# Kernel tuning notes

Hardware: AMD Instinct MI355X
Metric: run time of the kernel (lower is better)

## Reference

```python
import jax, jax.numpy as jnp
import numpy as np

B, N, H = 2, 2048, 1024
NUM_HEADS, HEAD_DIM = 16, 64
SCALE = HEAD_DIM ** -0.5


def setup_inputs() -> dict:
    key = jax.random.key(0)
    ks = jax.random.split(key, 9)
    hidden_states = jax.random.normal(ks[0], (B, N, H), dtype=jnp.float32)
    # ancestor-only mask: lower-triangular incl. diagonal (chain tree)
    tree_mask = jnp.tril(jnp.ones((N, N), dtype=jnp.int32))
    s = H ** -0.5
    Wq = jax.random.normal(ks[1], (H, NUM_HEADS * HEAD_DIM), dtype=jnp.float32) * s
    Wk = jax.random.normal(ks[2], (H, NUM_HEADS * HEAD_DIM), dtype=jnp.float32) * s
    Wv = jax.random.normal(ks[3], (H, NUM_HEADS * HEAD_DIM), dtype=jnp.float32) * s
    Wo = jax.random.normal(ks[4], (NUM_HEADS * HEAD_DIM, H), dtype=jnp.float32) * s
    bq = jnp.zeros((NUM_HEADS * HEAD_DIM,), dtype=jnp.float32)
    bk = jnp.zeros((NUM_HEADS * HEAD_DIM,), dtype=jnp.float32)
    bv = jnp.zeros((NUM_HEADS * HEAD_DIM,), dtype=jnp.float32)
    bo = jnp.zeros((H,), dtype=jnp.float32)
    return {"hidden_states": hidden_states, "tree_mask": tree_mask,
            "Wq": Wq, "bq": bq, "Wk": Wk, "bk": bk,
            "Wv": Wv, "bv": bv, "Wo": Wo, "bo": bo}


def reference(hidden_states, tree_mask, Wq, bq, Wk, bk, Wv, bv, Wo, bo):
    b, n, _ = hidden_states.shape
    q = (hidden_states @ Wq + bq).reshape(b, n, NUM_HEADS, HEAD_DIM)
    k = (hidden_states @ Wk + bk).reshape(b, n, NUM_HEADS, HEAD_DIM)
    v = (hidden_states @ Wv + bv).reshape(b, n, NUM_HEADS, HEAD_DIM)
    # scores: [b, heads, n, n]
    scores = jnp.einsum('bqhd,bkhd->bhqk', q, k) * SCALE
    neg_inf = jnp.finfo(scores.dtype).min
    scores = jnp.where(tree_mask[None, None, :, :] == 0, neg_inf, scores)
    attn = jax.nn.softmax(scores, axis=-1)  # dropout p=0.0 -> identity
    out = jnp.einsum('bhqk,bkhd->bqhd', attn, v).reshape(b, n, NUM_HEADS * HEAD_DIM)
    return out @ Wo + bo
```

## Files before the change

kernel.cpp:

```cpp
#include <hip/hip_runtime.h>
#include <hip/hip_bf16.h>
#include <stdint.h>

typedef unsigned short u16;
typedef short short8 __attribute__((ext_vector_type(8)));
typedef float f32x4 __attribute__((ext_vector_type(4)));
typedef u16 u16x4 __attribute__((ext_vector_type(4)));

#define SCLOG 0.18033688011112042f

static __device__ __forceinline__ u16 f2bf(float f) {
  unsigned u = __float_as_uint(f);
  unsigned rnd = 0x7fffu + ((u >> 16) & 1u);
  return (u16)((u + rnd) >> 16);
}

static __device__ __forceinline__ unsigned pk_bf16(float a, float b) {
  unsigned r;
  asm("v_cvt_pk_bf16_f32 %0, %1, %2" : "=v"(r) : "v"(a), "v"(b));
  return r;
}

static __device__ __forceinline__ void gload_lds16(const void* g, void* l) {
  __builtin_amdgcn_global_load_lds(
      (const __attribute__((address_space(1))) unsigned int*)g,
      (__attribute__((address_space(3))) unsigned int*)l, 16, 0, 0);
}

__global__ __launch_bounds__(256) void cvt_hs_kernel(const float4* __restrict__ src,
                                                     u16x4* __restrict__ dst) {
  int i = blockIdx.x * 256 + threadIdx.x;
  float4 v = src[i];
  u16x4 o;
  o[0] = f2bf(v.x); o[1] = f2bf(v.y); o[2] = f2bf(v.z); o[3] = f2bf(v.w);
  dst[i] = o;
}

__global__ __launch_bounds__(256) void cvt_transpose_kernel(
    const float* __restrict__ Wq, const float* __restrict__ Wk,
    const float* __restrict__ Wv, const float* __restrict__ Wo,
    u16* __restrict__ WT) {
  __shared__ float tile[32][33];
  const int z = blockIdx.z;
  const float* src = (z == 0) ? Wq : (z == 1) ? Wk : (z == 2) ? Wv : Wo;
  u16* dst = WT + (size_t)z * 1024 * 1024;
  const int row0 = blockIdx.y * 32, col0 = blockIdx.x * 32;
  const int tx = threadIdx.x, ty = threadIdx.y;
#pragma unroll
  for (int i = 0; i < 4; ++i)
    tile[ty + i * 8][tx] = src[(size_t)(row0 + ty + i * 8) * 1024 + col0 + tx];
  __syncthreads();
#pragma unroll
  for (int i = 0; i < 4; ++i) {
    int r = ty + i * 8;
    dst[(size_t)(col0 + r) * 1024 + row0 + tx] = f2bf(tile[tx][r]);
  }
}

__global__ __launch_bounds__(256) void mask_bits_kernel(const int* __restrict__ mask,
                                                        unsigned long long* __restrict__ bits) {
  int gw = blockIdx.x * 4 + (threadIdx.x >> 6);
  int lane = threadIdx.x & 63;
  int q = gw >> 5, w = gw & 31;
  int mv = mask[(size_t)q * 2048 + w * 64 + lane];
  unsigned long long bal = __ballot(mv != 0);
  if (lane == 0) bits[(size_t)q * 32 + w] = bal;
}

__global__ __launch_bounds__(256) void gemm_qkv_kernel(
    const u16* __restrict__ X, const u16* __restrict__ WT,
    const float* __restrict__ bq, const float* __restrict__ bk, const float* __restrict__ bv,
    u16* __restrict__ Qb, u16* __restrict__ Kb, u16* __restrict__ Vb) {
  __shared__ u16 As[128 * 32];
  __shared__ u16 Bs[128 * 32];
  const int tid = threadIdx.x;
  const int lane = tid & 63, wid = tid >> 6;
  const int l15 = lane & 15, lg = lane >> 4;
  const int n0 = blockIdx.x * 128, m0 = blockIdx.y * 128;
  const int wr = wid >> 1, wc = wid & 1;

  f32x4 acc[4][4] = {};

  for (int kt = 0; kt < 32; ++kt) {
    __syncthreads();
#pragma unroll
    for (int p = 0; p < 2; ++p) {
      const int c = p * 256 + tid;
      const int r = c >> 2, ch = c & 3;
      gload_lds16(X + (size_t)(m0 + r) * 1024 + kt * 32 + ch * 8,
                  &As[(p * 256 + wid * 64) * 8]);
      gload_lds16(WT + (size_t)(n0 + r) * 1024 + kt * 32 + ch * 8,
                  &Bs[(p * 256 + wid * 64) * 8]);
    }
    __syncthreads();
    short8 af[4], bfr[4];
#pragma unroll
    for (int i = 0; i < 4; ++i) {
      af[i] = *reinterpret_cast<const short8*>(&As[(wr * 64 + i * 16 + l15) * 32 + lg * 8]);
      bfr[i] = *reinterpret_cast<const short8*>(&Bs[(wc * 64 + i * 16 + l15) * 32 + lg * 8]);
    }
#pragma unroll
    for (int i = 0; i < 4; ++i)
#pragma unroll
      for (int j = 0; j < 4; ++j)
        acc[i][j] = __builtin_amdgcn_mfma_f32_16x16x32_bf16(af[i], bfr[j], acc[i][j], 0, 0, 0);
  }

#pragma unroll
  for (int j = 0; j < 4; ++j) {
    const int n = n0 + wc * 64 + j * 16 + l15;
    const float bias = (n < 1024) ? bq[n] : (n < 2048) ? bk[n - 1024] : bv[n - 2048];
    const float scl = (n < 1024) ? SCLOG : 1.0f;
    u16* dst = (n < 1024) ? Qb : (n < 2048) ? Kb : Vb;
    const int nl = n & 1023;
    const int hh = nl >> 6, d = nl & 63;
#pragma unroll
    for (int i = 0; i < 4; ++i) {
#pragma unroll
      for (int r = 0; r < 4; ++r) {
        const int m = m0 + wr * 64 + i * 16 + lg * 4 + r;
        const int bb = m >> 11, t = m & 2047;
        dst[((size_t)(bb * 16 + hh) * 2048 + t) * 64 + d] = f2bf((acc[i][j][r] + bias) * scl);
      }
    }
  }
}

__global__ __launch_bounds__(256) void transpose_v_kernel(const u16* __restrict__ Vb,
                                                          u16* __restrict__ VT) {
  __shared__ u16 tile[64][68];
  const int tid = threadIdx.x;
  const int tt = blockIdx.x & 31;
  const int bh = blockIdx.x >> 5;
  const size_t base = (size_t)bh * 2048 * 64;
  const int t0 = tt * 64;
#pragma unroll
  for (int p = 0; p < 2; ++p) {
    int i = p * 256 + tid;
    int row = i >> 3, ch = i & 7;
    *reinterpret_cast<short8*>(&tile[row][ch * 8]) =
        *reinterpret_cast<const short8*>(Vb + base + (size_t)(t0 + row) * 64 + ch * 8);
  }
  __syncthreads();
#pragma unroll
  for (int p = 0; p < 2; ++p) {
    int i = p * 256 + tid;
    int d = i >> 3, ch = i & 7;
    short8 v;
#pragma unroll
    for (int j = 0; j < 8; ++j) v[j] = tile[ch * 8 + j][d];
    *reinterpret_cast<short8*>(VT + base + (size_t)d * 2048 + t0 + ch * 8) = v;
  }
}

struct AttnState {
  f32x4 O[4];
  float m, l;
  short8 qf0, qf1;
};

static __device__ __forceinline__ void attn_tile(
    AttnState& st, const u16* __restrict__ Kb_, const u16* __restrict__ Vb_,
    u16* __restrict__ pwave, unsigned long long w,
    int l15, int lg, int slg) {
  f32x4 sT[4] = {};
  __builtin_amdgcn_s_setprio(1);
#pragma unroll
  for (int dc = 0; dc < 2; ++dc) {
    const short8 qv = dc ? st.qf1 : st.qf0;
#pragma unroll
    for (int sub = 0; sub < 4; ++sub) {
      const short8 kf = *reinterpret_cast<const short8*>(
          &Kb_[dc * 2048 + (sub * 16 + l15) * 32 + slg]);
      sT[sub] = __builtin_amdgcn_mfma_f32_16x16x32_bf16(kf, qv, sT[sub], 0, 0, 0);
    }
  }
  __builtin_amdgcn_s_setprio(0);

  float pm = -3e38f;
  if (__all(w == ~0ull)) {
#pragma unroll
    for (int sub = 0; sub < 4; ++sub)
#pragma unroll
      for (int r = 0; r < 4; ++r) pm = fmaxf(pm, sT[sub][r]);
  } else {
    const unsigned mlo = (unsigned)w, mhi = (unsigned)(w >> 32);
#pragma unroll
    for (int sub = 0; sub < 4; ++sub) {
      const unsigned f = ((sub & 2) ? mhi : mlo) >> ((sub & 1) * 16 + lg * 4);
#pragma unroll
      for (int r = 0; r < 4; ++r) {
        const float val = ((f >> r) & 1u) ? sT[sub][r] : -1e30f;
        sT[sub][r] = val;
        pm = fmaxf(pm, val);
      }
    }
  }
  pm = fmaxf(pm, __shfl_xor(pm, 16));
  pm = fmaxf(pm, __shfl_xor(pm, 32));
  if (!__all(pm - st.m <= 8.f)) {
    const float mn = fmaxf(st.m, pm);
    const float al = exp2f(st.m - mn);
    st.m = mn;
    st.l *= al;
#pragma unroll
    for (int dt = 0; dt < 4; ++dt) st.O[dt] *= al;
  }

  float lsum = 0.f;
#pragma unroll
  for (int kc = 0; kc < 2; ++kc) {
#pragma unroll
    for (int s2 = 0; s2 < 2; ++s2) {
      const int sub = kc * 2 + s2;
      const float e0 = exp2f(sT[sub][0] - st.m);
      const float e1 = exp2f(sT[sub][1] - st.m);
      const float e2 = exp2f(sT[sub][2] - st.m);
      const float e3 = exp2f(sT[sub][3] - st.m);
      lsum += (e0 + e1) + (e2 + e3);
      uint2 pk;
      pk.x = pk_bf16(e0, e1);
      pk.y = pk_bf16(e2, e3);
      *reinterpret_cast<uint2*>(&pwave[l15 * 40 + s2 * 16 + lg * 4]) = pk;
    }
    const short8 pf = *reinterpret_cast<const short8*>(&pwave[l15 * 40 + lg * 8]);
    __builtin_amdgcn_s_setprio(1);
#pragma unroll
    for (int dt = 0; dt < 4; ++dt) {
      const short8 vf = *reinterpret_cast<const short8*>(
          &Vb_[kc * 2048 + (dt * 16 + l15) * 32 + slg]);
      st.O[dt] = __builtin_amdgcn_mfma_f32_16x16x32_bf16(vf, pf, st.O[dt], 0, 0, 0);
    }
    __builtin_amdgcn_s_setprio(0);
  }
  lsum += __shfl_xor(lsum, 16);
  lsum += __shfl_xor(lsum, 32);
  st.l += lsum;
}

__global__ __launch_bounds__(256, 4) void attn_kernel(
    const u16* __restrict__ Q, const u16* __restrict__ K, const u16* __restrict__ VT,
    const unsigned long long* __restrict__ MB, u16* __restrict__ AO) {
  __shared__ u16 K_lds[2][4096];
  __shared__ u16 V_lds[2][4096];
  __shared__ u16 p_lds[4][16][40];
  __shared__ unsigned actA_s, actB_s;

  const int tid = threadIdx.x;
  const int wid = tid >> 6, lane = tid & 63;
  const int l15 = lane & 15, lg = lane >> 4;

  const int qp = blockIdx.x;
  const int qA_t = qp, qB_t = 31 - qp;
  const int h = blockIdx.y;
  const int b = blockIdx.z;
  const size_t bh_off = ((size_t)(b * 16 + h)) * 2048 * 64;

  if (tid == 0) { actA_s = 0; actB_s = 0; }
  __syncthreads();
  {
    const int ktc = tid & 31, qg = tid >> 5;
    unsigned long long orA = 0, orB = 0;
#pragma unroll
    for (int i = 0; i < 8; ++i) {
      orA |= MB[(size_t)(qA_t * 64 + qg * 8 + i) * 32 + ktc];
      orB |= MB[(size_t)(qB_t * 64 + qg * 8 + i) * 32 + ktc];
    }
    if (orA) atomicOr(&actA_s, 1u << ktc);
    if (orB) atomicOr(&actB_s, 1u << ktc);
  }

  const int qa = qA_t * 64 + wid * 16 + l15;
  const int qb = qB_t * 64 + wid * 16 + l15;

  AttnState stA, stB;
  {
    const short8* qpA = reinterpret_cast<const short8*>(Q + bh_off + (size_t)qa * 64);
    const short8* qpB = reinterpret_cast<const short8*>(Q + bh_off + (size_t)qb * 64);
    stA.qf0 = qpA[lg]; stA.qf1 = qpA[4 + lg];
    stB.qf0 = qpB[lg]; stB.qf1 = qpB[4 + lg];
#pragma unroll
    for (int dt = 0; dt < 4; ++dt) { stA.O[dt] = f32x4{}; stB.O[dt] = f32x4{}; }
    stA.m = -3e38f; stA.l = 0.f;
    stB.m = -3e38f; stB.l = 0.f;
  }

  const int slg = (lg ^ ((l15 >> 1) & 3)) * 8;

  int offK[2], offV[2], ldsi[2];
#pragma unroll
  for (int p = 0; p < 2; ++p) {
    const int i = wid * 128 + p * 64 + lane;
    const int pc = i >> 8, row = (i >> 2) & 63, lgc = i & 3;
    const int lgs = lgc ^ ((i >> 3) & 3);
    offK[p] = row * 64 + pc * 32 + lgs * 8;
    offV[p] = row * 2048 + pc * 32 + lgs * 8;
    ldsi[p] = (wid * 128 + p * 64) * 8;
  }
  const u16* Kg = K + bh_off;
  const u16* Vg = VT + bh_off;
  u16* pwave = &p_lds[wid][0][0];

  __syncthreads();
  const unsigned actA = actA_s, actB = actB_s;
  unsigned rem = actA | actB;
  int buf = 0;

#define STAGE_TILE(bb, ktv)                                        \
  do {                                                             \
    const u16* ksrc_ = Kg + (ktv) * 64 * 64;                       \
    const u16* vsrc_ = Vg + (ktv) * 64;                            \
    _Pragma("unroll") for (int p_ = 0; p_ < 2; ++p_) {             \
      gload_lds16(ksrc_ + offK[p_], &K_lds[bb][ldsi[p_]]);         \
      gload_lds16(vsrc_ + offV[p_], &V_lds[bb][ldsi[p_]]);         \
    }                                                              \
  } while (0)

  if (rem) {
    int kt = __ffs(rem) - 1;
    unsigned long long wA_cur = MB[(size_t)qa * 32 + kt];
    unsigned long long wB_cur = MB[(size_t)qb * 32 + kt];
    STAGE_TILE(0, kt);
    __syncthreads();

    while (true) {
      rem &= rem - 1;
      int ktn = -1;
      unsigned long long wA_next = 0, wB_next = 0;
      if (rem) {
        ktn = __ffs(rem) - 1;
        wA_next = MB[(size_t)qa * 32 + ktn];
        wB_next = MB[(size_t)qb * 32 + ktn];
        STAGE_TILE(buf ^ 1, ktn);
      }

      if ((actB >> kt) & 1u)
        attn_tile(stB, &K_lds[buf][0], &V_lds[buf][0], pwave, wB_cur, l15, lg, slg);
      if ((actA >> kt) & 1u)
        attn_tile(stA, &K_lds[buf][0], &V_lds[buf][0], pwave, wA_cur, l15, lg, slg);

      if (ktn < 0) break;
      __syncthreads();
      buf ^= 1;
      kt = ktn;
      wA_cur = wA_next;
      wB_cur = wB_next;
    }
  }
#undef STAGE_TILE

  {
    const float invA = (stA.l > 0.f) ? (1.0f / stA.l) : 0.f;
    u16* dstA = AO + ((size_t)(b * 2048 + qa)) * 1024 + h * 64;
#pragma unroll
    for (int dt = 0; dt < 4; ++dt) {
      uint2 pk;
      pk.x = pk_bf16(stA.O[dt][0] * invA, stA.O[dt][1] * invA);
      pk.y = pk_bf16(stA.O[dt][2] * invA, stA.O[dt][3] * invA);
      *reinterpret_cast<uint2*>(dstA + dt * 16 + lg * 4) = pk;
    }
    const float invB = (stB.l > 0.f) ? (1.0f / stB.l) : 0.f;
    u16* dstB = AO + ((size_t)(b * 2048 + qb)) * 1024 + h * 64;
#pragma unroll
    for (int dt = 0; dt < 4; ++dt) {
      uint2 pk;
      pk.x = pk_bf16(stB.O[dt][0] * invB, stB.O[dt][1] * invB);
      pk.y = pk_bf16(stB.O[dt][2] * invB, stB.O[dt][3] * invB);
      *reinterpret_cast<uint2*>(dstB + dt * 16 + lg * 4) = pk;
    }
  }
}

__global__ __launch_bounds__(256) void gemm_out_kernel(
    const u16* __restrict__ A, const u16* __restrict__ BT,
    const float* __restrict__ bo, float* __restrict__ out) {
  __shared__ u16 As[128 * 32];
  __shared__ u16 Bs[128 * 32];
  const int tid = threadIdx.x;
  const int lane = tid & 63, wid = tid >> 6;
  const int l15 = lane & 15, lg = lane >> 4;
  const int n0 = blockIdx.x * 128, m0 = blockIdx.y * 128;
  const int wr = wid >> 1, wc = wid & 1;

  f32x4 acc[4][4] = {};

  for (int kt = 0; kt < 32; ++kt) {
    __syncthreads();
#pragma unroll
    for (int p = 0; p < 2; ++p) {
      const int c = p * 256 + tid;
      const int r = c >> 2, ch = c & 3;
      gload_lds16(A + (size_t)(m0 + r) * 1024 + kt * 32 + ch * 8,
                  &As[(p * 256 + wid * 64) * 8]);
      gload_lds16(BT + (size_t)(n0 + r) * 1024 + kt * 32 + ch * 8,
                  &Bs[(p * 256 + wid * 64) * 8]);
    }
    __syncthreads();
    short8 af[4], bfr[4];
#pragma unroll
    for (int i = 0; i < 4; ++i) {
      af[i] = *reinterpret_cast<const short8*>(&As[(wr * 64 + i * 16 + l15) * 32 + lg * 8]);
      bfr[i] = *reinterpret_cast<const short8*>(&Bs[(wc * 64 + i * 16 + l15) * 32 + lg * 8]);
    }
#pragma unroll
    for (int i = 0; i < 4; ++i)
#pragma unroll
      for (int j = 0; j < 4; ++j)
        acc[i][j] = __builtin_amdgcn_mfma_f32_16x16x32_bf16(af[i], bfr[j], acc[i][j], 0, 0, 0);
  }

#pragma unroll
  for (int j = 0; j < 4; ++j) {
    const int n = n0 + wc * 64 + j * 16 + l15;
    const float bias = bo[n];
#pragma unroll
    for (int i = 0; i < 4; ++i)
#pragma unroll
      for (int r = 0; r < 4; ++r) {
        const int m = m0 + wr * 64 + i * 16 + lg * 4 + r;
        out[(size_t)m * 1024 + n] = acc[i][j][r] + bias;
      }
  }
}

extern "C" void kernel_launch(void* const* d_in, const int* in_sizes, int n_in,
                              void* d_out, int out_size, void* d_ws, size_t ws_size,
                              hipStream_t stream) {
  (void)in_sizes; (void)n_in; (void)out_size; (void)ws_size;
  const float* hs = (const float*)d_in[0];
  const int* mask = (const int*)d_in[1];
  const float* Wq = (const float*)d_in[2];
  const float* bq = (const float*)d_in[3];
  const float* Wk = (const float*)d_in[4];
  const float* bk = (const float*)d_in[5];
  const float* Wv = (const float*)d_in[6];
  const float* bv = (const float*)d_in[7];
  const float* Wo = (const float*)d_in[8];
  const float* bo = (const float*)d_in[9];
  float* out = (float*)d_out;

  uint8_t* ws = (uint8_t*)d_ws;
  u16* X  = (u16*)(ws);
  u16* WT = (u16*)(ws + ((size_t)8 << 20));
  u16* Qb = (u16*)(ws + ((size_t)16 << 20));
  u16* Kb = (u16*)(ws + ((size_t)24 << 20));
  u16* Vb = (u16*)(ws + ((size_t)32 << 20));
  u16* AO = (u16*)(ws + ((size_t)40 << 20));
  unsigned long long* MB = (unsigned long long*)(ws + ((size_t)48 << 20));
  u16* VbT = X;

  cvt_hs_kernel<<<dim3(4096), dim3(256), 0, stream>>>((const float4*)hs, (u16x4*)X);
  cvt_transpose_kernel<<<dim3(32, 32, 4), dim3(32, 8), 0, stream>>>(Wq, Wk, Wv, Wo, WT);
  mask_bits_kernel<<<dim3(16384), dim3(256), 0, stream>>>(mask, MB);
  gemm_qkv_kernel<<<dim3(24, 32), dim3(256), 0, stream>>>(X, WT, bq, bk, bv, Qb, Kb, Vb);
  transpose_v_kernel<<<dim3(1024), dim3(256), 0, stream>>>(Vb, VbT);
  attn_kernel<<<dim3(16, 16, 2), dim3(256), 0, stream>>>(Qb, Kb, VbT, MB, AO);
  gemm_out_kernel<<<dim3(8, 32), dim3(256), 0, stream>>>(AO, WT + (size_t)3072 * 1024, bo, out);
}
```

Baseline: 159.2 us.

## Merge prep kernels into one launch and vectorize GEMM epilogue stores

The three preprocessing kernels (hidden-state bf16 conversion, weight transpose-convert, mask bit packing) are folded into a single launch that dispatches on block index, which removes two kernel launches and their gaps. The MFMA operand order in both GEMMs is also swapped so each lane holds four consecutive output columns. This lets the epilogue issue 8-byte packed bf16 stores and float4 output stores with vector bias loads, in place of scattered scalar stores. The cost is a __syncthreads inside a divergent branch of the merged kernel, which is safe only because the whole block takes the same branch.

```diff
diff --git a/kernel.cpp b/kernel.cpp
--- a/kernel.cpp
+++ b/kernel.cpp
@@ -27,44 +27,45 @@
       (__attribute__((address_space(3))) unsigned int*)l, 16, 0, 0);
 }
 
-__global__ __launch_bounds__(256) void cvt_hs_kernel(const float4* __restrict__ src,
-                                                     u16x4* __restrict__ dst) {
-  int i = blockIdx.x * 256 + threadIdx.x;
-  float4 v = src[i];
-  u16x4 o;
-  o[0] = f2bf(v.x); o[1] = f2bf(v.y); o[2] = f2bf(v.z); o[3] = f2bf(v.w);
-  dst[i] = o;
-}
-
-__global__ __launch_bounds__(256) void cvt_transpose_kernel(
+__global__ __launch_bounds__(256) void prep_kernel(
+    const float* __restrict__ hs, const int* __restrict__ mask,
     const float* __restrict__ Wq, const float* __restrict__ Wk,
     const float* __restrict__ Wv, const float* __restrict__ Wo,
-    u16* __restrict__ WT) {
+    u16* __restrict__ X, u16* __restrict__ WT,
+    unsigned long long* __restrict__ bits) {
   __shared__ float tile[32][33];
-  const int z = blockIdx.z;
-  const float* src = (z == 0) ? Wq : (z == 1) ? Wk : (z == 2) ? Wv : Wo;
-  u16* dst = WT + (size_t)z * 1024 * 1024;
-  const int row0 = blockIdx.y * 32, col0 = blockIdx.x * 32;
-  const int tx = threadIdx.x, ty = threadIdx.y;
-#pragma unroll
-  for (int i = 0; i < 4; ++i)
-    tile[ty + i * 8][tx] = src[(size_t)(row0 + ty + i * 8) * 1024 + col0 + tx];
-  __syncthreads();
-#pragma unroll
-  for (int i = 0; i < 4; ++i) {
-    int r = ty + i * 8;
-    dst[(size_t)(col0 + r) * 1024 + row0 + tx] = f2bf(tile[tx][r]);
-  }
-}
-
-__global__ __launch_bounds__(256) void mask_bits_kernel(const int* __restrict__ mask,
-                                                        unsigned long long* __restrict__ bits) {
-  int gw = blockIdx.x * 4 + (threadIdx.x >> 6);
-  int lane = threadIdx.x & 63;
-  int q = gw >> 5, w = gw & 31;
-  int mv = mask[(size_t)q * 2048 + w * 64 + lane];
-  unsigned long long bal = __ballot(mv != 0);
-  if (lane == 0) bits[(size_t)q * 32 + w] = bal;
+  const int bid = blockIdx.x;
+  const int tid = threadIdx.x;
+  if (bid < 4096) {
+    const int i = bid * 256 + tid;
+    const float4 v = reinterpret_cast<const float4*>(hs)[i];
+    u16x4 o;
+    o[0] = f2bf(v.x); o[1] = f2bf(v.y); o[2] = f2bf(v.z); o[3] = f2bf(v.w);
+    reinterpret_cast<u16x4*>(X)[i] = o;
+  } else if (bid < 8192) {
+    const int B = bid - 4096;
+    const int z = B >> 10, y = (B >> 5) & 31, x = B & 31;
+    const float* src = (z == 0) ? Wq : (z == 1) ? Wk : (z == 2) ? Wv : Wo;
+    u16* dst = WT + (size_t)z * 1024 * 1024;
+    const int row0 = y * 32, col0 = x * 32;
+    const int tx = tid & 31, ty = tid >> 5;
+#pragma unroll
+    for (int i = 0; i < 4; ++i)
+      tile[ty + i * 8][tx] = src[(size_t)(row0 + ty + i * 8) * 1024 + col0 + tx];
+    __syncthreads();
+#pragma unroll
+    for (int i = 0; i < 4; ++i) {
+      const int r = ty + i * 8;
+      dst[(size_t)(col0 + r) * 1024 + row0 + tx] = f2bf(tile[tx][r]);
+    }
+  } else {
+    const int gw = (bid - 8192) * 4 + (tid >> 6);
+    const int lane = tid & 63;
+    const int q = gw >> 5, w = gw & 31;
+    const int mv = mask[(size_t)q * 2048 + w * 64 + lane];
+    const unsigned long long bal = __ballot(mv != 0);
+    if (lane == 0) bits[(size_t)q * 32 + w] = bal;
+  }
 }
 
 __global__ __launch_bounds__(256) void gemm_qkv_kernel(
@@ -103,25 +104,26 @@
     for (int i = 0; i < 4; ++i)
 #pragma unroll
       for (int j = 0; j < 4; ++j)
-        acc[i][j] = __builtin_amdgcn_mfma_f32_16x16x32_bf16(af[i], bfr[j], acc[i][j], 0, 0, 0);
-  }
-
-#pragma unroll
-  for (int j = 0; j < 4; ++j) {
-    const int n = n0 + wc * 64 + j * 16 + l15;
-    const float bias = (n < 1024) ? bq[n] : (n < 2048) ? bk[n - 1024] : bv[n - 2048];
-    const float scl = (n < 1024) ? SCLOG : 1.0f;
-    u16* dst = (n < 1024) ? Qb : (n < 2048) ? Kb : Vb;
-    const int nl = n & 1023;
-    const int hh = nl >> 6, d = nl & 63;
-#pragma unroll
-    for (int i = 0; i < 4; ++i) {
-#pragma unroll
-      for (int r = 0; r < 4; ++r) {
-        const int m = m0 + wr * 64 + i * 16 + lg * 4 + r;
-        const int bb = m >> 11, t = m & 2047;
-        dst[((size_t)(bb * 16 + hh) * 2048 + t) * 64 + d] = f2bf((acc[i][j][r] + bias) * scl);
-      }
+        acc[i][j] = __builtin_amdgcn_mfma_f32_16x16x32_bf16(bfr[j], af[i], acc[i][j], 0, 0, 0);
+  }
+
+#pragma unroll
+  for (int i = 0; i < 4; ++i) {
+    const int m = m0 + wr * 64 + i * 16 + l15;
+    const int bb = m >> 11, t = m & 2047;
+#pragma unroll
+    for (int j = 0; j < 4; ++j) {
+      const int n = n0 + wc * 64 + j * 16 + lg * 4;
+      const float* bsrc = (n < 1024) ? (bq + n) : (n < 2048) ? (bk + n - 1024) : (bv + n - 2048);
+      const float4 b4 = *reinterpret_cast<const float4*>(bsrc);
+      const float scl = (n < 1024) ? SCLOG : 1.0f;
+      u16* dst = (n < 1024) ? Qb : (n < 2048) ? Kb : Vb;
+      const int nl = n & 1023;
+      const int hh = nl >> 6, d0 = nl & 63;
+      uint2 pk;
+      pk.x = pk_bf16((acc[i][j][0] + b4.x) * scl, (acc[i][j][1] + b4.y) * scl);
+      pk.y = pk_bf16((acc[i][j][2] + b4.z) * scl, (acc[i][j][3] + b4.w) * scl);
+      *reinterpret_cast<uint2*>(dst + ((size_t)(bb * 16 + hh) * 2048 + t) * 64 + d0) = pk;
     }
   }
 }
@@ -406,20 +408,23 @@
     for (int i = 0; i < 4; ++i)
 #pragma unroll
       for (int j = 0; j < 4; ++j)
-        acc[i][j] = __builtin_amdgcn_mfma_f32_16x16x32_bf16(af[i], bfr[j], acc[i][j], 0, 0, 0);
-  }
-
-#pragma unroll
-  for (int j = 0; j < 4; ++j) {
-    const int n = n0 + wc * 64 + j * 16 + l15;
-    const float bias = bo[n];
-#pragma unroll
-    for (int i = 0; i < 4; ++i)
-#pragma unroll
-      for (int r = 0; r < 4; ++r) {
-        const int m = m0 + wr * 64 + i * 16 + lg * 4 + r;
-        out[(size_t)m * 1024 + n] = acc[i][j][r] + bias;
-      }
+        acc[i][j] = __builtin_amdgcn_mfma_f32_16x16x32_bf16(bfr[j], af[i], acc[i][j], 0, 0, 0);
+  }
+
+#pragma unroll
+  for (int i = 0; i < 4; ++i) {
+    const int m = m0 + wr * 64 + i * 16 + l15;
+#pragma unroll
+    for (int j = 0; j < 4; ++j) {
+      const int n = n0 + wc * 64 + j * 16 + lg * 4;
+      const float4 b4 = *reinterpret_cast<const float4*>(bo + n);
+      float4 o4;
+      o4.x = acc[i][j][0] + b4.x;
+      o4.y = acc[i][j][1] + b4.y;
+      o4.z = acc[i][j][2] + b4.z;
+      o4.w = acc[i][j][3] + b4.w;
+      *reinterpret_cast<float4*>(out + (size_t)m * 1024 + n) = o4;
+    }
   }
 }
 
@@ -449,9 +454,7 @@
   unsigned long long* MB = (unsigned long long*)(ws + ((size_t)48 << 20));
   u16* VbT = X;
 
-  cvt_hs_kernel<<<dim3(4096), dim3(256), 0, stream>>>((const float4*)hs, (u16x4*)X);
-  cvt_transpose_kernel<<<dim3(32, 32, 4), dim3(32, 8), 0, stream>>>(Wq, Wk, Wv, Wo, WT);
-  mask_bits_kernel<<<dim3(16384), dim3(256), 0, stream>>>(mask, MB);
+  prep_kernel<<<dim3(24576), dim3(256), 0, stream>>>(hs, mask, Wq, Wk, Wv, Wo, X, WT, MB);
   gemm_qkv_kernel<<<dim3(24, 32), dim3(256), 0, stream>>>(X, WT, bq, bk, bv, Qb, Kb, Vb);
   transpose_v_kernel<<<dim3(1024), dim3(256), 0, stream>>>(Vb, VbT);
   attn_kernel<<<dim3(16, 16, 2), dim3(256), 0, stream>>>(Qb, Kb, VbT, MB, AO);
```

Result: faster. 146.9 us (-7.7%).
